# Performance work log

Measured on AMD Instinct MI355X. Metric: run time of the kernel, lower is better.

The kernel has to match this reference:

```python
import jax, jax.numpy as jnp
import numpy as np

BN_EPS = 1e-5

def _square_distance(src, dst):
    # src [B,N,3], dst [B,S,3] -> [B,N,S]
    d = -2.0 * jnp.einsum('bnc,bsc->bns', src, dst)
    d = d + jnp.sum(src * src, -1)[:, :, None]
    d = d + jnp.sum(dst * dst, -1)[:, None, :]
    return d

def _conv_bn_relu(x, w, b, g, beta):
    # x [B,C,N]; 1x1 conv == channel GEMM, then training-mode batchnorm over (B,N)
    y = jnp.einsum('oc,bcn->bon', w, x) + b[None, :, None]
    mean = jnp.mean(y, axis=(0, 2), keepdims=True)
    var = jnp.mean((y - mean) ** 2, axis=(0, 2), keepdims=True)  # biased, as torch BN uses for normalization
    y = (y - mean) * jax.lax.rsqrt(var + BN_EPS)
    y = y * g[None, :, None] + beta[None, :, None]
    return jax.nn.relu(y)

def setup_inputs() -> dict:
    key = jax.random.key(0)
    ks = jax.random.split(key, 8)
    B, N, S, D1, D2 = 8, 8192, 2048, 128, 256
    C_in, C_mid, C_out = D1 + D2, 256, 256
    return {
        'xyz1': jax.random.normal(ks[0], (B, 3, N), jnp.float32),
        'xyz2': jax.random.normal(ks[1], (B, 3, S), jnp.float32),
        'points1': jax.random.normal(ks[2], (B, D1, N), jnp.float32),
        'points2': jax.random.normal(ks[3], (B, D2, S), jnp.float32),
        'w1': jax.random.normal(ks[4], (C_mid, C_in), jnp.float32) * (1.0 / np.sqrt(C_in)),
        'b1': jax.random.normal(ks[5], (C_mid,), jnp.float32) * 0.01,
        'g1': jnp.ones((C_mid,), jnp.float32),
        'beta1': jnp.zeros((C_mid,), jnp.float32),
        'w2': jax.random.normal(ks[6], (C_out, C_mid), jnp.float32) * (1.0 / np.sqrt(C_mid)),
        'b2': jax.random.normal(ks[7], (C_out,), jnp.float32) * 0.01,
        'g2': jnp.ones((C_out,), jnp.float32),
        'beta2': jnp.zeros((C_out,), jnp.float32),
    }

def reference(xyz1, xyz2, points1, points2, w1, b1, g1, beta1, w2, b2, g2, beta2):
    B = xyz1.shape[0]
    p1xyz = jnp.transpose(xyz1, (0, 2, 1))      # [B,N,3]
    p2xyz = jnp.transpose(xyz2, (0, 2, 1))      # [B,S,3]
    p2 = jnp.transpose(points2, (0, 2, 1))      # [B,S,D2]

    dists = _square_distance(p1xyz, p2xyz)      # [B,N,S]
    neg_d3, idx = jax.lax.top_k(-dists, 3)      # 3 smallest distances
    d3 = -neg_d3                                # [B,N,3]
    recip = 1.0 / (d3 + 1e-8)
    weight = recip / jnp.sum(recip, axis=2, keepdims=True)  # [B,N,3]

    gathered = jax.vmap(lambda p, i: p[i])(p2, idx)          # [B,N,3,D2]
    interp = jnp.sum(gathered * weight[..., None], axis=2)   # [B,N,D2]

    new_points = jnp.concatenate([jnp.transpose(points1, (0, 2, 1)), interp], axis=-1)
    x = jnp.transpose(new_points, (0, 2, 1))    # [B,D1+D2,N]
    x = _conv_bn_relu(x, w1, b1, g1, beta1)
    x = _conv_bn_relu(x, w2, b2, g2, beta2)
    return x
```

## Files before the change

kernel.cpp:

```cpp
#include <hip/hip_runtime.h>

#define B_    8
#define N_    8192
#define S_    2048
#define D1_   128
#define D2_   256
#define CIN_  384
#define CMID_ 256
#define COUT_ 256

typedef unsigned int  u32;
typedef unsigned short u16;
typedef __attribute__((ext_vector_type(8))) short short8;
typedef __attribute__((ext_vector_type(4))) float f32x4;

static __device__ __forceinline__ u32 uminu(u32 a, u32 b) { return a < b ? a : b; }
static __device__ __forceinline__ u32 umaxu(u32 a, u32 b) { return a > b ? a : b; }
static __device__ __forceinline__ u32 umed3(u32 a, u32 b, u32 c) {
  return umaxu(uminu(a, b), uminu(umaxu(a, b), c));
}
static __device__ __forceinline__ u16 f2bf(float f) {
  union { float f; u32 u; } v; v.f = f;
  u32 r = v.u + 0x7FFFu + ((v.u >> 16) & 1u);
  return (u16)(r >> 16);
}
static __device__ __forceinline__ float bflo(u32 u) { return __uint_as_float(u << 16); }
static __device__ __forceinline__ float bfhi(u32 u) { return __uint_as_float(u & 0xFFFF0000u); }

#define GLD16(g, l)                                                             \
  __builtin_amdgcn_global_load_lds((const __attribute__((address_space(1))) void*)(g), \
                                   (__attribute__((address_space(3))) void*)(l), 16, 0, 0)

__global__ __launch_bounds__(256) void k_prep(const float* __restrict__ xyz2,
                                              float4* __restrict__ pts4) {
  const int b = blockIdx.y, s = blockIdx.x * 256 + threadIdx.x;
  const float* xb = xyz2 + (size_t)b * 3 * S_;
  float x = xb[s], y = xb[S_ + s], z = xb[2 * S_ + s];
  pts4[b * S_ + s] = make_float4(-2.f * x, -2.f * y, -2.f * z, x * x + y * y + z * z);
}

__global__ __launch_bounds__(256) void k_nn_scan(const float* __restrict__ xyz1,
                                                 const float4* __restrict__ pts4,
                                                 uint4* __restrict__ keys) {
  const int b = blockIdx.z, chunk = blockIdx.y;
  const int n = blockIdx.x * 256 + threadIdx.x;
  const float* pb = xyz1 + (size_t)b * 3 * N_;
  const float px = pb[n], py = pb[N_ + n], pz = pb[2 * N_ + n];
  const float pn = px * px + py * py + pz * pz;
  const float4* __restrict__ P = pts4 + b * S_ + chunk * 256;
  u32 m0 = ~0u, m1 = ~0u, m2 = ~0u, m3 = ~0u;
#pragma unroll 8
  for (int s = 0; s < 256; ++s) {
    float4 q = P[s];
    float d = fmaf(px, q.x, fmaf(py, q.y, fmaf(pz, q.z, pn + q.w)));
    d = fmaxf(d, 0.f);
    u32 k = (__float_as_uint(d) & 0xFFFFFF00u) | (u32)s;
    m3 = uminu(m3, umaxu(m2, k));
    m2 = umed3(m1, m2, k);
    m1 = umed3(m0, m1, k);
    m0 = uminu(m0, k);
  }
  uint4 v; v.x = m0; v.y = m1; v.z = m2; v.w = m3;
  keys[((size_t)(b * 8 + chunk)) * N_ + n] = v;
}

__global__ __launch_bounds__(256) void k_refine(const float* __restrict__ xyz1,
                                                const float4* __restrict__ pts4,
                                                const uint4* __restrict__ keys,
                                                int4* __restrict__ idx4,
                                                float4* __restrict__ w4) {
  const int b = blockIdx.y, n = blockIdx.x * 256 + threadIdx.x;
  const float* pb = xyz1 + (size_t)b * 3 * N_;
  const double px = (double)pb[n], py = (double)pb[N_ + n], pz = (double)pb[2 * N_ + n];
  const double pn = px * px + py * py + pz * pz;
  double bd0 = 1e300, bd1 = 1e300, bd2 = 1e300;
  int bi0 = 1 << 30, bi1 = 1 << 30, bi2 = 1 << 30;
#pragma unroll
  for (int c = 0; c < 8; ++c) {
    uint4 kk = keys[((size_t)(b * 8 + c)) * N_ + n];
    u32 arr[4] = {kk.x, kk.y, kk.z, kk.w};
#pragma unroll
    for (int j = 0; j < 4; ++j) {
      int s = c * 256 + (int)(arr[j] & 255u);
      float4 q = pts4[b * S_ + s];
      double x = (double)(q.x * -0.5f), y = (double)(q.y * -0.5f), z = (double)(q.z * -0.5f);
      double dot = px * x + py * y + pz * z;
      double d = -2.0 * dot + (pn + (x * x + y * y + z * z));
      if (d < bd2 || (d == bd2 && s < bi2)) {
        if (d < bd1 || (d == bd1 && s < bi1)) {
          bd2 = bd1; bi2 = bi1;
          if (d < bd0 || (d == bd0 && s < bi0)) { bd1 = bd0; bi1 = bi0; bd0 = d; bi0 = s; }
          else                                  { bd1 = d;  bi1 = s; }
        } else { bd2 = d; bi2 = s; }
      }
    }
  }
  float f0 = (float)bd0, f1 = (float)bd1, f2 = (float)bd2;
  float r0 = 1.f / (f0 + 1e-8f), r1 = 1.f / (f1 + 1e-8f), r2 = 1.f / (f2 + 1e-8f);
  float rs = r0 + r1 + r2;
  w4[(size_t)b * N_ + n]   = make_float4(r0 / rs, r1 / rs, r2 / rs, 0.f);
  idx4[(size_t)b * N_ + n] = make_int4(bi0, bi1, bi2, 0);
}

__global__ __launch_bounds__(256) void k_p2t(const float* __restrict__ p2,
                                             float* __restrict__ p2T) {
  __shared__ float t[32][33];
  const int b = blockIdx.z, s0 = blockIdx.x * 32, d0 = blockIdx.y * 32;
  const int cc = threadIdx.x & 31, rr = threadIdx.x >> 5;
#pragma unroll
  for (int i = 0; i < 4; ++i) {
    int r = rr + i * 8;
    t[r][cc] = p2[((size_t)b * D2_ + d0 + r) * S_ + s0 + cc];
  }
  __syncthreads();
#pragma unroll
  for (int i = 0; i < 4; ++i) {
    int r = rr + i * 8;
    p2T[((size_t)b * S_ + s0 + r) * D2_ + d0 + cc] = t[cc][r];
  }
}

__global__ __launch_bounds__(256) void k_packp1(const float* __restrict__ p1,
                                                u16* __restrict__ xT) {
  __shared__ float t[32][33];
  const int b = blockIdx.z, n0 = blockIdx.x * 32, c0 = blockIdx.y * 32;
  const int cc = threadIdx.x & 31, rr = threadIdx.x >> 5;
#pragma unroll
  for (int i = 0; i < 4; ++i) {
    int r = rr + i * 8;
    t[r][cc] = p1[((size_t)b * D1_ + c0 + r) * N_ + n0 + cc];
  }
  __syncthreads();
#pragma unroll
  for (int i = 0; i < 4; ++i) {
    int r = rr + i * 8;
    xT[((size_t)b * N_ + n0 + r) * CIN_ + c0 + cc] = f2bf(t[cc][r]);
  }
}

__global__ __launch_bounds__(256) void k_gather_pack(const float* __restrict__ p2T,
                                                     const int4* __restrict__ idx4,
                                                     const float4* __restrict__ w4,
                                                     u16* __restrict__ xT) {
  const int b = blockIdx.y;
  const int wv = threadIdx.x >> 6, lane = threadIdx.x & 63;
  const int nbase = blockIdx.x * 16 + wv * 4;
  int4   id[4];
  float4 w[4];
#pragma unroll
  for (int i = 0; i < 4; ++i) {
    id[i] = idx4[(size_t)b * N_ + nbase + i];
    w[i]  = w4[(size_t)b * N_ + nbase + i];
  }
#pragma unroll
  for (int i = 0; i < 4; ++i) {
    const int n = nbase + i;
    const float4* r0 = (const float4*)(p2T + ((size_t)b * S_ + id[i].x) * D2_) + lane;
    const float4* r1 = (const float4*)(p2T + ((size_t)b * S_ + id[i].y) * D2_) + lane;
    const float4* r2 = (const float4*)(p2T + ((size_t)b * S_ + id[i].z) * D2_) + lane;
    float4 a = *r0, bb = *r1, cq = *r2;
    ushort4 pk;
    pk.x = f2bf(a.x * w[i].x + bb.x * w[i].y + cq.x * w[i].z);
    pk.y = f2bf(a.y * w[i].x + bb.y * w[i].y + cq.y * w[i].z);
    pk.z = f2bf(a.z * w[i].x + bb.z * w[i].y + cq.z * w[i].z);
    pk.w = f2bf(a.w * w[i].x + bb.w * w[i].y + cq.w * w[i].z);
    *(ushort4*)(xT + ((size_t)b * N_ + n) * CIN_ + D1_ + lane * 4) = pk;
  }
}

__global__ __launch_bounds__(256) void k_wcvt(const float* __restrict__ w1,
                                              const float* __restrict__ w2,
                                              u16* __restrict__ w1b,
                                              u16* __restrict__ w2b) {
  int i = blockIdx.x * 256 + threadIdx.x;
  if (i < CMID_ * CIN_) w1b[i] = f2bf(w1[i]);
  int j = i - CMID_ * CIN_;
  if (j >= 0 && j < COUT_ * CMID_) w2b[j] = f2bf(w2[j]);
}

__global__ __launch_bounds__(256) void k_gemm1(const u16* __restrict__ Wb,
                                               const float* __restrict__ bias,
                                               const u16* __restrict__ xT,
                                               u16* __restrict__ y1T,
                                               float* __restrict__ sum,
                                               float* __restrict__ sumsq) {
  __shared__ u16 As[128 * 32];
  __shared__ u16 Bs[128 * 32];
  __shared__ float s_sum[128], s_ssq[128];
  const int b = blockIdx.z, bm0 = blockIdx.y * 128, bn0 = blockIdx.x * 128;
  const int tid = threadIdx.x, w = tid >> 6, l = tid & 63;
  const int wm = w & 1, wn = w >> 1;
  const int lr = l >> 2, lc = l & 3;
  const int fm = l & 15, fq = l >> 4;
  if (tid < 128) { s_sum[tid] = 0.f; s_ssq[tid] = 0.f; }
  f32x4 acc[4][4];
#pragma unroll
  for (int i = 0; i < 4; ++i)
#pragma unroll
    for (int j = 0; j < 4; ++j) acc[i][j] = (f32x4){0.f, 0.f, 0.f, 0.f};

  for (int k0 = 0; k0 < CIN_; k0 += 32) {
    __syncthreads();
#pragma unroll
    for (int j = 0; j < 2; ++j) {
      int seg = w * 2 + j;
      int row = seg * 16 + lr;
      const u16* ga = Wb + (size_t)(bm0 + row) * CIN_ + k0 + lc * 8;
      const u16* gb = xT + ((size_t)b * N_ + bn0 + row) * CIN_ + k0 + lc * 8;
      GLD16(ga, &As[seg * 512]);
      GLD16(gb, &Bs[seg * 512]);
    }
    __syncthreads();
    short8 af[4], bfr[4];
#pragma unroll
    for (int f = 0; f < 4; ++f) {
      af[f]  = *(const short8*)&As[(wm * 64 + f * 16 + fm) * 32 + fq * 8];
      bfr[f] = *(const short8*)&Bs[(wn * 64 + f * 16 + fm) * 32 + fq * 8];
    }
#pragma unroll
    for (int i = 0; i < 4; ++i)
#pragma unroll
      for (int j = 0; j < 4; ++j)
        acc[i][j] = __builtin_amdgcn_mfma_f32_16x16x32_bf16(af[i], bfr[j], acc[i][j], 0, 0, 0);
  }
#pragma unroll
  for (int i = 0; i < 4; ++i) {
    int ob = bm0 + wm * 64 + i * 16 + fq * 4;
    float4 b4 = *(const float4*)(bias + ob);
    float sv0 = 0, sv1 = 0, sv2 = 0, sv3 = 0, qv0 = 0, qv1 = 0, qv2 = 0, qv3 = 0;
#pragma unroll
    for (int j = 0; j < 4; ++j) {
      int n = bn0 + wn * 64 + j * 16 + fm;
      ushort4 pk;
      pk.x = f2bf(acc[i][j][0] + b4.x);
      pk.y = f2bf(acc[i][j][1] + b4.y);
      pk.z = f2bf(acc[i][j][2] + b4.z);
      pk.w = f2bf(acc[i][j][3] + b4.w);
      *(ushort4*)(y1T + ((size_t)b * N_ + n) * CMID_ + ob) = pk;
      float v0 = bflo(pk.x), v1 = bflo(pk.y), v2 = bflo(pk.z), v3 = bflo(pk.w);
      sv0 += v0; sv1 += v1; sv2 += v2; sv3 += v3;
      qv0 = fmaf(v0, v0, qv0); qv1 = fmaf(v1, v1, qv1);
      qv2 = fmaf(v2, v2, qv2); qv3 = fmaf(v3, v3, qv3);
    }
#pragma unroll
    for (int m = 1; m <= 8; m <<= 1) {
      sv0 += __shfl_xor(sv0, m); sv1 += __shfl_xor(sv1, m);
      sv2 += __shfl_xor(sv2, m); sv3 += __shfl_xor(sv3, m);
      qv0 += __shfl_xor(qv0, m); qv1 += __shfl_xor(qv1, m);
      qv2 += __shfl_xor(qv2, m); qv3 += __shfl_xor(qv3, m);
    }
    if (fm == 0) {
      int ol = wm * 64 + i * 16 + fq * 4;
      atomicAdd(&s_sum[ol + 0], sv0); atomicAdd(&s_sum[ol + 1], sv1);
      atomicAdd(&s_sum[ol + 2], sv2); atomicAdd(&s_sum[ol + 3], sv3);
      atomicAdd(&s_ssq[ol + 0], qv0); atomicAdd(&s_ssq[ol + 1], qv1);
      atomicAdd(&s_ssq[ol + 2], qv2); atomicAdd(&s_ssq[ol + 3], qv3);
    }
  }
  __syncthreads();
  if (tid < 128) {
    atomicAdd(&sum[bm0 + tid], s_sum[tid]);
    atomicAdd(&sumsq[bm0 + tid], s_ssq[tid]);
  }
}

__global__ __launch_bounds__(256) void k_affine(const float* __restrict__ sum,
                                                const float* __restrict__ sumsq,
                                                const float* __restrict__ g,
                                                const float* __restrict__ beta,
                                                float* __restrict__ scale,
                                                float* __restrict__ shift) {
  int o = threadIdx.x;
  const float inv = 1.0f / (float)(B_ * N_);
  float m = sum[o] * inv;
  float var = sumsq[o] * inv - m * m;
  float sc = g[o] / sqrtf(var + 1e-5f);
  scale[o] = sc;
  shift[o] = beta[o] - m * sc;
}

__global__ __launch_bounds__(256) void k_gemm2(const u16* __restrict__ Wb2,
                                               const float* __restrict__ b2,
                                               const u16* __restrict__ y1T,
                                               const float* __restrict__ scale,
                                               const float* __restrict__ shift,
                                               u16* __restrict__ y2T,
                                               float* __restrict__ sum,
                                               float* __restrict__ sumsq) {
  __shared__ u16 As[128 * 32];
  __shared__ u16 Bs[128 * 32];
  __shared__ float s_sum[128], s_ssq[128];
  const int b = blockIdx.z, bm0 = blockIdx.y * 128, bn0 = blockIdx.x * 128;
  const int tid = threadIdx.x, w = tid >> 6, l = tid & 63;
  const int wm = w & 1, wn = w >> 1;
  const int lr = l >> 2, lc = l & 3;
  const int fm = l & 15, fq = l >> 4;
  if (tid < 128) { s_sum[tid] = 0.f; s_ssq[tid] = 0.f; }
  f32x4 acc[4][4];
#pragma unroll
  for (int i = 0; i < 4; ++i)
#pragma unroll
    for (int j = 0; j < 4; ++j) acc[i][j] = (f32x4){0.f, 0.f, 0.f, 0.f};

  for (int k0 = 0; k0 < CMID_; k0 += 32) {
    __syncthreads();
#pragma unroll
    for (int j = 0; j < 2; ++j) {
      int seg = w * 2 + j;
      int row = seg * 16 + lr;
      const u16* ga = Wb2 + (size_t)(bm0 + row) * CMID_ + k0 + lc * 8;
      GLD16(ga, &As[seg * 512]);
    }
#pragma unroll
    for (int i = 0; i < 2; ++i) {
      int li = tid + i * 256;
      int n = li >> 2, cp = li & 3;
      int c = k0 + cp * 8;
      uint4 r = *(const uint4*)(y1T + ((size_t)b * N_ + bn0 + n) * CMID_ + c);
      float4 sA = *(const float4*)(scale + c);
      float4 sB = *(const float4*)(scale + c + 4);
      float4 hA = *(const float4*)(shift + c);
      float4 hB = *(const float4*)(shift + c + 4);
      float v0 = fmaxf(fmaf(bflo(r.x), sA.x, hA.x), 0.f);
      float v1 = fmaxf(fmaf(bfhi(r.x), sA.y, hA.y), 0.f);
      float v2 = fmaxf(fmaf(bflo(r.y), sA.z, hA.z), 0.f);
      float v3 = fmaxf(fmaf(bfhi(r.y), sA.w, hA.w), 0.f);
      float v4 = fmaxf(fmaf(bflo(r.z), sB.x, hB.x), 0.f);
      float v5 = fmaxf(fmaf(bfhi(r.z), sB.y, hB.y), 0.f);
      float v6 = fmaxf(fmaf(bflo(r.w), sB.z, hB.z), 0.f);
      float v7 = fmaxf(fmaf(bfhi(r.w), sB.w, hB.w), 0.f);
      uint4 pk;
      pk.x = (u32)f2bf(v0) | ((u32)f2bf(v1) << 16);
      pk.y = (u32)f2bf(v2) | ((u32)f2bf(v3) << 16);
      pk.z = (u32)f2bf(v4) | ((u32)f2bf(v5) << 16);
      pk.w = (u32)f2bf(v6) | ((u32)f2bf(v7) << 16);
      *(uint4*)&Bs[n * 32 + cp * 8] = pk;
    }
    __syncthreads();
    short8 af[4], bfr[4];
#pragma unroll
    for (int f = 0; f < 4; ++f) {
      af[f]  = *(const short8*)&As[(wm * 64 + f * 16 + fm) * 32 + fq * 8];
      bfr[f] = *(const short8*)&Bs[(wn * 64 + f * 16 + fm) * 32 + fq * 8];
    }
#pragma unroll
    for (int i = 0; i < 4; ++i)
#pragma unroll
      for (int j = 0; j < 4; ++j)
        acc[i][j] = __builtin_amdgcn_mfma_f32_16x16x32_bf16(af[i], bfr[j], acc[i][j], 0, 0, 0);
  }
#pragma unroll
  for (int i = 0; i < 4; ++i) {
    int ob = bm0 + wm * 64 + i * 16 + fq * 4;
    float4 b4 = *(const float4*)(b2 + ob);
    float sv0 = 0, sv1 = 0, sv2 = 0, sv3 = 0, qv0 = 0, qv1 = 0, qv2 = 0, qv3 = 0;
#pragma unroll
    for (int j = 0; j < 4; ++j) {
      int n = bn0 + wn * 64 + j * 16 + fm;
      ushort4 pk;
      pk.x = f2bf(acc[i][j][0] + b4.x);
      pk.y = f2bf(acc[i][j][1] + b4.y);
      pk.z = f2bf(acc[i][j][2] + b4.z);
      pk.w = f2bf(acc[i][j][3] + b4.w);
      *(ushort4*)(y2T + ((size_t)b * N_ + n) * COUT_ + ob) = pk;
      float v0 = bflo(pk.x), v1 = bflo(pk.y), v2 = bflo(pk.z), v3 = bflo(pk.w);
      sv0 += v0; sv1 += v1; sv2 += v2; sv3 += v3;
      qv0 = fmaf(v0, v0, qv0); qv1 = fmaf(v1, v1, qv1);
      qv2 = fmaf(v2, v2, qv2); qv3 = fmaf(v3, v3, qv3);
    }
#pragma unroll
    for (int m = 1; m <= 8; m <<= 1) {
      sv0 += __shfl_xor(sv0, m); sv1 += __shfl_xor(sv1, m);
      sv2 += __shfl_xor(sv2, m); sv3 += __shfl_xor(sv3, m);
      qv0 += __shfl_xor(qv0, m); qv1 += __shfl_xor(qv1, m);
      qv2 += __shfl_xor(qv2, m); qv3 += __shfl_xor(qv3, m);
    }
    if (fm == 0) {
      int ol = wm * 64 + i * 16 + fq * 4;
      atomicAdd(&s_sum[ol + 0], sv0); atomicAdd(&s_sum[ol + 1], sv1);
      atomicAdd(&s_sum[ol + 2], sv2); atomicAdd(&s_sum[ol + 3], sv3);
      atomicAdd(&s_ssq[ol + 0], qv0); atomicAdd(&s_ssq[ol + 1], qv1);
      atomicAdd(&s_ssq[ol + 2], qv2); atomicAdd(&s_ssq[ol + 3], qv3);
    }
  }
  __syncthreads();
  if (tid < 128) {
    atomicAdd(&sum[bm0 + tid], s_sum[tid]);
    atomicAdd(&sumsq[bm0 + tid], s_ssq[tid]);
  }
}

__global__ __launch_bounds__(256) void k_bn2t(const u16* __restrict__ y2T,
                                              const float* __restrict__ scale,
                                              const float* __restrict__ shift,
                                              float* __restrict__ out) {
  __shared__ float t[32][33];
  const int b = blockIdx.z, n0 = blockIdx.x * 32, o0 = blockIdx.y * 32;
  const int cc = threadIdx.x & 31, rr = threadIdx.x >> 5;
  const float sc = scale[o0 + cc], sh = shift[o0 + cc];
#pragma unroll
  for (int i = 0; i < 4; ++i) {
    int r = rr + i * 8;
    float v = bflo((u32)y2T[((size_t)b * N_ + n0 + r) * COUT_ + o0 + cc]);
    t[r][cc] = fmaxf(fmaf(v, sc, sh), 0.f);
  }
  __syncthreads();
#pragma unroll
  for (int i = 0; i < 4; ++i) {
    int r = rr + i * 8;
    out[((size_t)b * COUT_ + o0 + r) * N_ + n0 + cc] = t[cc][r];
  }
}

extern "C" void kernel_launch(void* const* d_in, const int* in_sizes, int n_in,
                              void* d_out, int out_size, void* d_ws, size_t ws_size,
                              hipStream_t stream) {
  const float* xyz1    = (const float*)d_in[0];
  const float* xyz2    = (const float*)d_in[1];
  const float* points1 = (const float*)d_in[2];
  const float* points2 = (const float*)d_in[3];
  const float* w1      = (const float*)d_in[4];
  const float* b1      = (const float*)d_in[5];
  const float* g1      = (const float*)d_in[6];
  const float* beta1   = (const float*)d_in[7];
  const float* w2      = (const float*)d_in[8];
  const float* b2      = (const float*)d_in[9];
  const float* g2      = (const float*)d_in[10];
  const float* beta2   = (const float*)d_in[11];
  float* out = (float*)d_out;

  char* ws = (char*)d_ws;
  size_t off = 0;
  u16*    xT    = (u16*)(ws + off);    off += (size_t)B_ * N_ * CIN_ * 2;
  u16*    y1T   = (u16*)(ws + off);    off += (size_t)B_ * N_ * CMID_ * 2;
  float*  p2T   = (float*)(ws + off);  off += (size_t)B_ * S_ * D2_ * 4;
  float4* pts4  = (float4*)(ws + off); off += (size_t)B_ * S_ * 16;
  uint4*  keys  = (uint4*)(ws + off);  off += (size_t)B_ * 8 * N_ * 16;
  int4*   idx4  = (int4*)(ws + off);   off += (size_t)B_ * N_ * 16;
  float4* w4    = (float4*)(ws + off); off += (size_t)B_ * N_ * 16;
  u16*    w1b   = (u16*)(ws + off);    off += (size_t)CMID_ * CIN_ * 2;
  u16*    w2b   = (u16*)(ws + off);    off += (size_t)COUT_ * CMID_ * 2;
  float*  stats = (float*)(ws + off);
  u16*    y2T   = xT;

  hipMemsetAsync(stats, 0, 1024 * sizeof(float), stream);

  k_wcvt       <<<dim3((CMID_ * CIN_ + COUT_ * CMID_) / 256), 256, 0, stream>>>(w1, w2, w1b, w2b);
  k_prep       <<<dim3(S_ / 256, B_), 256, 0, stream>>>(xyz2, pts4);
  k_p2t        <<<dim3(S_ / 32, D2_ / 32, B_), 256, 0, stream>>>(points2, p2T);
  k_nn_scan    <<<dim3(N_ / 256, 8, B_), 256, 0, stream>>>(xyz1, pts4, keys);
  k_refine     <<<dim3(N_ / 256, B_), 256, 0, stream>>>(xyz1, pts4, keys, idx4, w4);
  k_packp1     <<<dim3(N_ / 32, D1_ / 32, B_), 256, 0, stream>>>(points1, xT);
  k_gather_pack<<<dim3(N_ / 16, B_), 256, 0, stream>>>(p2T, idx4, w4, xT);
  k_gemm1      <<<dim3(N_ / 128, CMID_ / 128, B_), 256, 0, stream>>>(w1b, b1, xT, y1T,
                                                                     stats + 0, stats + 256);
  k_affine     <<<1, 256, 0, stream>>>(stats + 0, stats + 256, g1, beta1, stats + 1024, stats + 1280);
  k_gemm2      <<<dim3(N_ / 128, COUT_ / 128, B_), 256, 0, stream>>>(w2b, b2, y1T,
                                                                     stats + 1024, stats + 1280,
                                                                     y2T, stats + 512, stats + 768);
  k_affine     <<<1, 256, 0, stream>>>(stats + 512, stats + 768, g2, beta2, stats + 1536, stats + 1792);
  k_bn2t       <<<dim3(N_ / 32, COUT_ / 32, B_), 256, 0, stream>>>(y2T, stats + 1536, stats + 1792, out);
}
```

Measured before the change: 299.0 us.

## Split NN top-4 insertion into two chains and XOR-swizzle GEMM LDS tiles

The nearest-neighbour scan now processes two candidates per iteration into two independent top-4 lists, merged at the end, which shortens the serial min/median dependency chain. Both GEMM kernels XOR-swizzle the 16-byte column segment in shared memory, by permuting the global source column for the direct-to-LDS loads and by permuting the store index in gemm2's B tile. This is meant to remove LDS bank conflicts on the short8 fragment reads. It adds a few integer ops per iteration and doubles the registers used for the top-4 keys.

```diff
diff --git a/kernel.cpp b/kernel.cpp
--- a/kernel.cpp
+++ b/kernel.cpp
@@ -48,19 +48,30 @@
   const float px = pb[n], py = pb[N_ + n], pz = pb[2 * N_ + n];
   const float pn = px * px + py * py + pz * pz;
   const float4* __restrict__ P = pts4 + b * S_ + chunk * 256;
-  u32 m0 = ~0u, m1 = ~0u, m2 = ~0u, m3 = ~0u;
+  u32 a0 = ~0u, a1 = ~0u, a2 = ~0u, a3 = ~0u;
+  u32 c0 = ~0u, c1 = ~0u, c2 = ~0u, c3 = ~0u;
 #pragma unroll 8
-  for (int s = 0; s < 256; ++s) {
-    float4 q = P[s];
-    float d = fmaf(px, q.x, fmaf(py, q.y, fmaf(pz, q.z, pn + q.w)));
-    d = fmaxf(d, 0.f);
-    u32 k = (__float_as_uint(d) & 0xFFFFFF00u) | (u32)s;
-    m3 = uminu(m3, umaxu(m2, k));
-    m2 = umed3(m1, m2, k);
-    m1 = umed3(m0, m1, k);
-    m0 = uminu(m0, k);
-  }
-  uint4 v; v.x = m0; v.y = m1; v.z = m2; v.w = m3;
+  for (int s = 0; s < 256; s += 2) {
+    float4 q0 = P[s], q1 = P[s + 1];
+    float d0 = fmaf(px, q0.x, fmaf(py, q0.y, fmaf(pz, q0.z, pn + q0.w)));
+    float d1 = fmaf(px, q1.x, fmaf(py, q1.y, fmaf(pz, q1.z, pn + q1.w)));
+    d0 = fmaxf(d0, 0.f);
+    d1 = fmaxf(d1, 0.f);
+    u32 k0 = (__float_as_uint(d0) & 0xFFFFFF00u) | (u32)s;
+    u32 k1 = (__float_as_uint(d1) & 0xFFFFFF00u) | (u32)(s + 1);
+    a3 = uminu(a3, umaxu(a2, k0)); a2 = umed3(a1, a2, k0);
+    a1 = umed3(a0, a1, k0);        a0 = uminu(a0, k0);
+    c3 = uminu(c3, umaxu(c2, k1)); c2 = umed3(c1, c2, k1);
+    c1 = umed3(c0, c1, k1);        c0 = uminu(c0, k1);
+  }
+  u32 mk[4] = {c0, c1, c2, c3};
+#pragma unroll
+  for (int j = 0; j < 4; ++j) {
+    u32 k = mk[j];
+    a3 = uminu(a3, umaxu(a2, k)); a2 = umed3(a1, a2, k);
+    a1 = umed3(a0, a1, k);        a0 = uminu(a0, k);
+  }
+  uint4 v; v.x = a0; v.y = a1; v.z = a2; v.w = a3;
   keys[((size_t)(b * 8 + chunk)) * N_ + n] = v;
 }
 
@@ -192,6 +203,8 @@
   const int wm = w & 1, wn = w >> 1;
   const int lr = l >> 2, lc = l & 3;
   const int fm = l & 15, fq = l >> 4;
+  const int clog = (lc ^ ((lr >> 1) & 3)) * 8;
+  const int swz8 = (fq ^ ((fm >> 1) & 3)) * 8;
   if (tid < 128) { s_sum[tid] = 0.f; s_ssq[tid] = 0.f; }
   f32x4 acc[4][4];
 #pragma unroll
@@ -205,8 +218,8 @@
     for (int j = 0; j < 2; ++j) {
       int seg = w * 2 + j;
       int row = seg * 16 + lr;
-      const u16* ga = Wb + (size_t)(bm0 + row) * CIN_ + k0 + lc * 8;
-      const u16* gb = xT + ((size_t)b * N_ + bn0 + row) * CIN_ + k0 + lc * 8;
+      const u16* ga = Wb + (size_t)(bm0 + row) * CIN_ + k0 + clog;
+      const u16* gb = xT + ((size_t)b * N_ + bn0 + row) * CIN_ + k0 + clog;
       GLD16(ga, &As[seg * 512]);
       GLD16(gb, &Bs[seg * 512]);
     }
@@ -214,8 +227,8 @@
     short8 af[4], bfr[4];
 #pragma unroll
     for (int f = 0; f < 4; ++f) {
-      af[f]  = *(const short8*)&As[(wm * 64 + f * 16 + fm) * 32 + fq * 8];
-      bfr[f] = *(const short8*)&Bs[(wn * 64 + f * 16 + fm) * 32 + fq * 8];
+      af[f]  = *(const short8*)&As[(wm * 64 + f * 16 + fm) * 32 + swz8];
+      bfr[f] = *(const short8*)&Bs[(wn * 64 + f * 16 + fm) * 32 + swz8];
     }
 #pragma unroll
     for (int i = 0; i < 4; ++i)
@@ -295,6 +308,8 @@
   const int wm = w & 1, wn = w >> 1;
   const int lr = l >> 2, lc = l & 3;
   const int fm = l & 15, fq = l >> 4;
+  const int clog = (lc ^ ((lr >> 1) & 3)) * 8;
+  const int swz8 = (fq ^ ((fm >> 1) & 3)) * 8;
   if (tid < 128) { s_sum[tid] = 0.f; s_ssq[tid] = 0.f; }
   f32x4 acc[4][4];
 #pragma unroll
@@ -308,7 +323,7 @@
     for (int j = 0; j < 2; ++j) {
       int seg = w * 2 + j;
       int row = seg * 16 + lr;
-      const u16* ga = Wb2 + (size_t)(bm0 + row) * CMID_ + k0 + lc * 8;
+      const u16* ga = Wb2 + (size_t)(bm0 + row) * CMID_ + k0 + clog;
       GLD16(ga, &As[seg * 512]);
     }
 #pragma unroll
@@ -334,14 +349,15 @@
       pk.y = (u32)f2bf(v2) | ((u32)f2bf(v3) << 16);
       pk.z = (u32)f2bf(v4) | ((u32)f2bf(v5) << 16);
       pk.w = (u32)f2bf(v6) | ((u32)f2bf(v7) << 16);
-      *(uint4*)&Bs[n * 32 + cp * 8] = pk;
+      int cph = cp ^ ((n >> 1) & 3);
+      *(uint4*)&Bs[n * 32 + cph * 8] = pk;
     }
     __syncthreads();
     short8 af[4], bfr[4];
 #pragma unroll
     for (int f = 0; f < 4; ++f) {
-      af[f]  = *(const short8*)&As[(wm * 64 + f * 16 + fm) * 32 + fq * 8];
-      bfr[f] = *(const short8*)&Bs[(wn * 64 + f * 16 + fm) * 32 + fq * 8];
+      af[f]  = *(const short8*)&As[(wm * 64 + f * 16 + fm) * 32 + swz8];
+      bfr[f] = *(const short8*)&Bs[(wn * 64 + f * 16 + fm) * 32 + swz8];
     }
 #pragma unroll
     for (int i = 0; i < 4; ++i)
```

New measurement: 299.9 us. Within noise of the previous version (+0.3%).

## Double-buffer LDS tiles with XOR swizzle in both channel GEMMs

Applied to the files above, without the earlier changes.

Both 1x1-conv GEMM kernels now keep two LDS buffers and prefetch the next K-slice while MFMAs run on the current one, dropping one barrier per iteration. The column layout in LDS is XOR-swizzled to reduce bank conflicts on the short8 fragment reads, and the med3 helper is forced to a single v_med3_u32 instruction. This doubles LDS use per block, which may lower occupancy. In gemm2 the loaded y1 values stay live in registers across the MFMA block before being normalised and stored.

```diff
diff --git a/kernel.cpp b/kernel.cpp
--- a/kernel.cpp
+++ b/kernel.cpp
@@ -17,7 +17,9 @@
 static __device__ __forceinline__ u32 uminu(u32 a, u32 b) { return a < b ? a : b; }
 static __device__ __forceinline__ u32 umaxu(u32 a, u32 b) { return a > b ? a : b; }
 static __device__ __forceinline__ u32 umed3(u32 a, u32 b, u32 c) {
-  return umaxu(uminu(a, b), uminu(umaxu(a, b), c));
+  u32 d;
+  asm("v_med3_u32 %0, %1, %2, %3" : "=v"(d) : "v"(a), "v"(b), "v"(c));
+  return d;
 }
 static __device__ __forceinline__ u16 f2bf(float f) {
   union { float f; u32 u; } v; v.f = f;
@@ -184,14 +186,16 @@
                                                u16* __restrict__ y1T,
                                                float* __restrict__ sum,
                                                float* __restrict__ sumsq) {
-  __shared__ u16 As[128 * 32];
-  __shared__ u16 Bs[128 * 32];
+  __shared__ u16 As[2][4096];
+  __shared__ u16 Bs[2][4096];
   __shared__ float s_sum[128], s_ssq[128];
   const int b = blockIdx.z, bm0 = blockIdx.y * 128, bn0 = blockIdx.x * 128;
   const int tid = threadIdx.x, w = tid >> 6, l = tid & 63;
   const int wm = w & 1, wn = w >> 1;
   const int lr = l >> 2, lc = l & 3;
   const int fm = l & 15, fq = l >> 4;
+  const int clog = (lc ^ ((lr >> 1) & 3)) * 8;
+  const int swz8 = (fq ^ ((fm >> 1) & 3)) * 8;
   if (tid < 128) { s_sum[tid] = 0.f; s_ssq[tid] = 0.f; }
   f32x4 acc[4][4];
 #pragma unroll
@@ -199,23 +203,30 @@
 #pragma unroll
     for (int j = 0; j < 4; ++j) acc[i][j] = (f32x4){0.f, 0.f, 0.f, 0.f};
 
-  for (int k0 = 0; k0 < CIN_; k0 += 32) {
+  const int NK = CIN_ / 32;
+#pragma unroll
+  for (int j = 0; j < 2; ++j) {
+    int seg = w * 2 + j, row = seg * 16 + lr;
+    GLD16(Wb + (size_t)(bm0 + row) * CIN_ + clog, &As[0][seg * 512]);
+    GLD16(xT + ((size_t)b * N_ + bn0 + row) * CIN_ + clog, &Bs[0][seg * 512]);
+  }
+  for (int kk = 0; kk < NK; ++kk) {
     __syncthreads();
-#pragma unroll
-    for (int j = 0; j < 2; ++j) {
-      int seg = w * 2 + j;
-      int row = seg * 16 + lr;
-      const u16* ga = Wb + (size_t)(bm0 + row) * CIN_ + k0 + lc * 8;
-      const u16* gb = xT + ((size_t)b * N_ + bn0 + row) * CIN_ + k0 + lc * 8;
-      GLD16(ga, &As[seg * 512]);
-      GLD16(gb, &Bs[seg * 512]);
-    }
-    __syncthreads();
+    const int cur = kk & 1;
+    if (kk + 1 < NK) {
+      const int k0 = (kk + 1) * 32, nxt = cur ^ 1;
+#pragma unroll
+      for (int j = 0; j < 2; ++j) {
+        int seg = w * 2 + j, row = seg * 16 + lr;
+        GLD16(Wb + (size_t)(bm0 + row) * CIN_ + k0 + clog, &As[nxt][seg * 512]);
+        GLD16(xT + ((size_t)b * N_ + bn0 + row) * CIN_ + k0 + clog, &Bs[nxt][seg * 512]);
+      }
+    }
     short8 af[4], bfr[4];
 #pragma unroll
     for (int f = 0; f < 4; ++f) {
-      af[f]  = *(const short8*)&As[(wm * 64 + f * 16 + fm) * 32 + fq * 8];
-      bfr[f] = *(const short8*)&Bs[(wn * 64 + f * 16 + fm) * 32 + fq * 8];
+      af[f]  = *(const short8*)&As[cur][(wm * 64 + f * 16 + fm) * 32 + swz8];
+      bfr[f] = *(const short8*)&Bs[cur][(wn * 64 + f * 16 + fm) * 32 + swz8];
     }
 #pragma unroll
     for (int i = 0; i < 4; ++i)
@@ -287,14 +298,20 @@
                                                u16* __restrict__ y2T,
                                                float* __restrict__ sum,
                                                float* __restrict__ sumsq) {
-  __shared__ u16 As[128 * 32];
-  __shared__ u16 Bs[128 * 32];
+  __shared__ u16 As[2][4096];
+  __shared__ u16 Bs[2][4096];
   __shared__ float s_sum[128], s_ssq[128];
   const int b = blockIdx.z, bm0 = blockIdx.y * 128, bn0 = blockIdx.x * 128;
   const int tid = threadIdx.x, w = tid >> 6, l = tid & 63;
   const int wm = w & 1, wn = w >> 1;
   const int lr = l >> 2, lc = l & 3;
   const int fm = l & 15, fq = l >> 4;
+  const int clog = (lc ^ ((lr >> 1) & 3)) * 8;
+  const int swz8 = (fq ^ ((fm >> 1) & 3)) * 8;
+  const int bn_0 = tid >> 2, bcp0 = tid & 3;
+  const int bn_1 = (tid + 256) >> 2, bcp1 = (tid + 256) & 3;
+  const int bph0 = (bcp0 ^ ((bn_0 >> 1) & 3)) * 8;
+  const int bph1 = (bcp1 ^ ((bn_1 >> 1) & 3)) * 8;
   if (tid < 128) { s_sum[tid] = 0.f; s_ssq[tid] = 0.f; }
   f32x4 acc[4][4];
 #pragma unroll
@@ -302,52 +319,70 @@
 #pragma unroll
     for (int j = 0; j < 4; ++j) acc[i][j] = (f32x4){0.f, 0.f, 0.f, 0.f};
 
-  for (int k0 = 0; k0 < CMID_; k0 += 32) {
+  const int NK = CMID_ / 32;
+
+  auto bn_pack = [&](uint4 r, int c) -> uint4 {
+    float4 sA = *(const float4*)(scale + c);
+    float4 sB = *(const float4*)(scale + c + 4);
+    float4 hA = *(const float4*)(shift + c);
+    float4 hB = *(const float4*)(shift + c + 4);
+    float v0 = fmaxf(fmaf(bflo(r.x), sA.x, hA.x), 0.f);
+    float v1 = fmaxf(fmaf(bfhi(r.x), sA.y, hA.y), 0.f);
+    float v2 = fmaxf(fmaf(bflo(r.y), sA.z, hA.z), 0.f);
+    float v3 = fmaxf(fmaf(bfhi(r.y), sA.w, hA.w), 0.f);
+    float v4 = fmaxf(fmaf(bflo(r.z), sB.x, hB.x), 0.f);
+    float v5 = fmaxf(fmaf(bfhi(r.z), sB.y, hB.y), 0.f);
+    float v6 = fmaxf(fmaf(bflo(r.w), sB.z, hB.z), 0.f);
+    float v7 = fmaxf(fmaf(bfhi(r.w), sB.w, hB.w), 0.f);
+    uint4 pk;
+    pk.x = (u32)f2bf(v0) | ((u32)f2bf(v1) << 16);
+    pk.y = (u32)f2bf(v2) | ((u32)f2bf(v3) << 16);
+    pk.z = (u32)f2bf(v4) | ((u32)f2bf(v5) << 16);
+    pk.w = (u32)f2bf(v6) | ((u32)f2bf(v7) << 16);
+    return pk;
+  };
+
+  {
+#pragma unroll
+    for (int j = 0; j < 2; ++j) {
+      int seg = w * 2 + j, row = seg * 16 + lr;
+      GLD16(Wb2 + (size_t)(bm0 + row) * CMID_ + clog, &As[0][seg * 512]);
+    }
+    uint4 r0 = *(const uint4*)(y1T + ((size_t)b * N_ + bn0 + bn_0) * CMID_ + bcp0 * 8);
+    uint4 r1 = *(const uint4*)(y1T + ((size_t)b * N_ + bn0 + bn_1) * CMID_ + bcp1 * 8);
+    *(uint4*)&Bs[0][bn_0 * 32 + bph0] = bn_pack(r0, bcp0 * 8);
+    *(uint4*)&Bs[0][bn_1 * 32 + bph1] = bn_pack(r1, bcp1 * 8);
+  }
+  for (int kk = 0; kk < NK; ++kk) {
     __syncthreads();
-#pragma unroll
-    for (int j = 0; j < 2; ++j) {
-      int seg = w * 2 + j;
-      int row = seg * 16 + lr;
-      const u16* ga = Wb2 + (size_t)(bm0 + row) * CMID_ + k0 + lc * 8;
-      GLD16(ga, &As[seg * 512]);
-    }
-#pragma unroll
-    for (int i = 0; i < 2; ++i) {
-      int li = tid + i * 256;
-      int n = li >> 2, cp = li & 3;
-      int c = k0 + cp * 8;
-      uint4 r = *(const uint4*)(y1T + ((size_t)b * N_ + bn0 + n) * CMID_ + c);
-      float4 sA = *(const float4*)(scale + c);
-      float4 sB = *(const float4*)(scale + c + 4);
-      float4 hA = *(const float4*)(shift + c);
-      float4 hB = *(const float4*)(shift + c + 4);
-      float v0 = fmaxf(fmaf(bflo(r.x), sA.x, hA.x), 0.f);
-      float v1 = fmaxf(fmaf(bfhi(r.x), sA.y, hA.y), 0.f);
-      float v2 = fmaxf(fmaf(bflo(r.y), sA.z, hA.z), 0.f);
-      float v3 = fmaxf(fmaf(bfhi(r.y), sA.w, hA.w), 0.f);
-      float v4 = fmaxf(fmaf(bflo(r.z), sB.x, hB.x), 0.f);
-      float v5 = fmaxf(fmaf(bfhi(r.z), sB.y, hB.y), 0.f);
-      float v6 = fmaxf(fmaf(bflo(r.w), sB.z, hB.z), 0.f);
-      float v7 = fmaxf(fmaf(bfhi(r.w), sB.w, hB.w), 0.f);
-      uint4 pk;
-      pk.x = (u32)f2bf(v0) | ((u32)f2bf(v1) << 16);
-      pk.y = (u32)f2bf(v2) | ((u32)f2bf(v3) << 16);
-      pk.z = (u32)f2bf(v4) | ((u32)f2bf(v5) << 16);
-      pk.w = (u32)f2bf(v6) | ((u32)f2bf(v7) << 16);
-      *(uint4*)&Bs[n * 32 + cp * 8] = pk;
-    }
-    __syncthreads();
+    const int cur = kk & 1;
+    uint4 r0, r1;
+    const bool have = (kk + 1 < NK);
+    const int k0n = (kk + 1) * 32, nxt = cur ^ 1;
+    if (have) {
+      r0 = *(const uint4*)(y1T + ((size_t)b * N_ + bn0 + bn_0) * CMID_ + k0n + bcp0 * 8);
+      r1 = *(const uint4*)(y1T + ((size_t)b * N_ + bn0 + bn_1) * CMID_ + k0n + bcp1 * 8);
+#pragma unroll
+      for (int j = 0; j < 2; ++j) {
+        int seg = w * 2 + j, row = seg * 16 + lr;
+        GLD16(Wb2 + (size_t)(bm0 + row) * CMID_ + k0n + clog, &As[nxt][seg * 512]);
+      }
+    }
     short8 af[4], bfr[4];
 #pragma unroll
     for (int f = 0; f < 4; ++f) {
-      af[f]  = *(const short8*)&As[(wm * 64 + f * 16 + fm) * 32 + fq * 8];
-      bfr[f] = *(const short8*)&Bs[(wn * 64 + f * 16 + fm) * 32 + fq * 8];
+      af[f]  = *(const short8*)&As[cur][(wm * 64 + f * 16 + fm) * 32 + swz8];
+      bfr[f] = *(const short8*)&Bs[cur][(wn * 64 + f * 16 + fm) * 32 + swz8];
     }
 #pragma unroll
     for (int i = 0; i < 4; ++i)
 #pragma unroll
       for (int j = 0; j < 4; ++j)
         acc[i][j] = __builtin_amdgcn_mfma_f32_16x16x32_bf16(af[i], bfr[j], acc[i][j], 0, 0, 0);
+    if (have) {
+      *(uint4*)&Bs[nxt][bn_0 * 32 + bph0] = bn_pack(r0, k0n + bcp0 * 8);
+      *(uint4*)&Bs[nxt][bn_1 * 32 + bph1] = bn_pack(r1, k0n + bcp1 * 8);
+    }
   }
 #pragma unroll
   for (int i = 0; i < 4; ++i) {
```

Result: no change. 295.7 us (-1.1%).
